# Kernel tuning notes

Hardware: AMD Instinct MI355X
Metric: run time of the kernel (lower is better)

Reference implementation:

```python
import jax, jax.numpy as jnp
import numpy as np

D_MODEL = 512
DQ = D_MODEL // 4  # 128
TIME_SHIFT_START = 256
VELOCITY_START = 768
NOTE_OFF_START = 128


def conv1d(x, w, b, stride, pad):
    # x: [B, Cin, L], w: [Cout, Cin, K]
    y = jax.lax.conv_general_dilated(x, w, (stride,), [(pad, pad)],
                                     dimension_numbers=('NCH', 'OIH', 'NCH'))
    return y + b[None, :, None]


def adaptive_avg_pool1d(x, out_size):
    # faithful to torch AdaptiveAvgPool1d bin boundaries
    L = x.shape[-1]
    starts = (np.arange(out_size) * L) // out_size
    ends = np.ceil((np.arange(out_size) + 1) * L / out_size).astype(np.int64)
    cs = jnp.concatenate([jnp.zeros(x.shape[:-1] + (1,), x.dtype),
                          jnp.cumsum(x, axis=-1)], axis=-1)
    return (cs[..., ends] - cs[..., starts]) / jnp.asarray(ends - starts, x.dtype)


def setup_inputs() -> dict:
    key = jax.random.key(0)
    ks = jax.random.split(key, 20)

    def w(k, shape):
        fan_in = int(np.prod(shape[1:]))
        return jax.random.normal(k, shape, jnp.float32) / np.sqrt(fan_in)

    def b(k, n):
        return jax.random.normal(k, (n,), jnp.float32) * 0.01

    return {
        'tokens': jax.random.randint(ks[0], (32, 4096), 0, 774),
        'r1_w': w(ks[1], (32, 1, 8)),    'r1_b': b(ks[2], 32),
        'r2_w': w(ks[3], (64, 32, 4)),   'r2_b': b(ks[4], 64),
        'h1_w': w(ks[5], (64, 128, 12)), 'h1_b': b(ks[6], 64),
        'h2_w': w(ks[7], (32, 64, 8)),   'h2_b': b(ks[8], 32),
        'm1_w': w(ks[9], (64, 128, 5)),  'm1_b': b(ks[10], 64),
        'm2_w': w(ks[11], (32, 64, 3)),  'm2_b': b(ks[12], 32),
        'd1_w': w(ks[13], (16, 6, 4)),   'd1_b': b(ks[14], 16),
        'd2_w': w(ks[15], (16, 16, 3)),  'd2_b': b(ks[16], 16),
        'fc_w': w(ks[17], (D_MODEL, D_MODEL)), 'fc_b': b(ks[18], D_MODEL),
    }


def reference(tokens, r1_w, r1_b, r2_w, r2_b, h1_w, h1_b, h2_w, h2_b,
              m1_w, m1_b, m2_w, m2_b, d1_w, d1_b, d2_w, d2_b, fc_w, fc_b):
    B, S = tokens.shape
    relu = jax.nn.relu

    # rhythm: binary time-shift indicator [B,1,S]
    ts = ((tokens >= TIME_SHIFT_START) & (tokens < VELOCITY_START)).astype(jnp.float32)[:, None, :]
    r = relu(conv1d(ts, r1_w, r1_b, 2, 3))
    r = relu(conv1d(r, r2_w, r2_b, 2, 1))
    r = adaptive_avg_pool1d(r, DQ).reshape(B, -1)  # [B, 64*DQ]

    # vectorized one-hot pitch scatter (replaces the python double loop): [B,128,S]
    nm = tokens < NOTE_OFF_START
    pitch = jnp.transpose(
        jax.nn.one_hot(jnp.where(nm, tokens, 0) % 128, 128, dtype=jnp.float32)
        * nm[..., None].astype(jnp.float32), (0, 2, 1))

    h = relu(conv1d(pitch, h1_w, h1_b, 1, 6))
    h = relu(conv1d(h, h2_w, h2_b, 2, 3))
    h = adaptive_avg_pool1d(h, DQ).reshape(B, -1)  # [B, 32*DQ]

    m = relu(conv1d(pitch, m1_w, m1_b, 1, 2))
    m = relu(conv1d(m, m2_w, m2_b, 1, 1))
    m = adaptive_avg_pool1d(m, DQ).reshape(B, -1)  # [B, 32*DQ]

    # velocity one-hot scatter: [B,6,S]
    vm = tokens >= VELOCITY_START
    vel = jnp.clip(jnp.where(vm, tokens - VELOCITY_START, 0), 0, 5)
    vpat = jnp.transpose(
        jax.nn.one_hot(vel, 6, dtype=jnp.float32) * vm[..., None].astype(jnp.float32),
        (0, 2, 1))
    d = relu(conv1d(vpat, d1_w, d1_b, 1, 2))
    d = relu(conv1d(d, d2_w, d2_b, 1, 1))
    d = adaptive_avg_pool1d(d, DQ).reshape(B, -1)  # [B, 16*DQ]

    # total flattened size is 36*d_model != d_model, so torch branch always pools
    r, h, m, d = [adaptive_avg_pool1d(f[:, None, :], DQ)[:, 0] for f in (r, h, m, d)]

    combined = jnp.concatenate([r, h, m, d], axis=1)       # [B, d_model]
    feats = combined @ fc_w.T + fc_b                        # Linear
    return jnp.broadcast_to(feats[:, None, :], (B, S, D_MODEL))
```

## Files before the change

### kernel.cpp

```cpp
#include <hip/hip_runtime.h>

typedef unsigned short u16;
typedef unsigned int u32;
typedef float vf4 __attribute__((ext_vector_type(4)));
typedef unsigned int vu4 __attribute__((ext_vector_type(4)));
typedef short sh8 __attribute__((ext_vector_type(8)));
typedef float f32x4 __attribute__((ext_vector_type(4)));

__device__ __forceinline__ float bf2f(u16 u) {
  return __uint_as_float(((u32)u) << 16);
}
__device__ __forceinline__ u16 f2bf(float f) {
  u32 x = __float_as_uint(f);
  return (u16)((x + 0x7fffu + ((x >> 16) & 1u)) >> 16);
}
__device__ __forceinline__ float ldin(const void* p, int idx, int isf) {
  return isf ? ((const float*)p)[idx] : bf2f(((const u16*)p)[idx]);
}

#define OFF_FLAG  ((size_t)0)
#define OFF_WB    ((size_t)16)
#define OFF_WTH1  ((size_t)1180432)
#define OFF_WTM1  ((size_t)1576720)
#define OFF_COMB  ((size_t)1741840)
#define OFF_FEATF ((size_t)1807376)
#define OFF_FEATB ((size_t)1872912)
#define OFF_DP    ((size_t)18686736)
#define OFF_WH2B  ((size_t)52536080)
#define OFF_WH2L  ((size_t)52568848)
#define OFF_WM2B  ((size_t)52601616)
#define OFF_WM2L  ((size_t)52613904)
#define WS_NEEDED ((size_t)52626192)

#define WB_R1W 0
#define WB_R1B 256
#define WB_R2W 288
#define WB_R2B 8480
#define WB_H1B 8544
#define WB_H2W 8608
#define WB_H2B 24992
#define WB_M1B 25024
#define WB_M2W 25088
#define WB_M2B 31232
#define WB_D1W 31264
#define WB_D1B 31648
#define WB_D2W 31664
#define WB_D2B 32432
#define WB_FCW 32448
#define WB_FCB 294592
#define WB_TOTAL 295104

#define CV_TH1_END 394176
#define CV_TM1_END 435456
#define CV_CMB_END 451840
#define CV_WH2_END 468224
#define CV_TOTAL   474368

__global__ __launch_bounds__(256) void k_convert(
    const void* r1_w, const void* r1_b, const void* r2_w, const void* r2_b,
    const void* h1_w, const void* h1_b, const void* h2_w, const void* h2_b,
    const void* m1_w, const void* m1_b, const void* m2_w, const void* m2_b,
    const void* d1_w, const void* d1_b, const void* d2_w, const void* d2_b,
    const void* fc_w, const void* fc_b,
    int* __restrict__ flagp, float* __restrict__ wb,
    float* __restrict__ wTh1, float* __restrict__ wTm1,
    float* __restrict__ combined,
    u16* __restrict__ wh2b, u16* __restrict__ wh2l,
    u16* __restrict__ wm2b, u16* __restrict__ wm2l) {
  __shared__ int cnt[4];
  int tid = threadIdx.x;
  {
    u16 v = ((const u16*)fc_w)[2 * tid];
    int e = (v >> 7) & 0xFF;
    int outside = (e < 100 || e > 140) ? 1 : 0;
    unsigned long long m = __ballot(outside);
    if ((tid & 63) == 0) cnt[tid >> 6] = __popcll(m);
  }
  __syncthreads();
  int isf = (cnt[0] + cnt[1] + cnt[2] + cnt[3] >= 64) ? 1 : 0;
  if (blockIdx.x == 0 && tid == 0) flagp[0] = isf;

  int j = blockIdx.x * 256 + tid;
  if (j >= CV_TOTAL) return;
  if (j < WB_TOTAL) {
    const void* src; int si;
    if      (j < WB_R1B) { src = r1_w; si = j; }
    else if (j < WB_R2W) { src = r1_b; si = j - WB_R1B; }
    else if (j < WB_R2B) { src = r2_w; si = j - WB_R2W; }
    else if (j < WB_H1B) { src = r2_b; si = j - WB_R2B; }
    else if (j < WB_H2W) { src = h1_b; si = j - WB_H1B; }
    else if (j < WB_H2B) { src = h2_w; si = j - WB_H2W; }
    else if (j < WB_M1B) { src = h2_b; si = j - WB_H2B; }
    else if (j < WB_M2W) { src = m1_b; si = j - WB_M1B; }
    else if (j < WB_M2B) { src = m2_w; si = j - WB_M2W; }
    else if (j < WB_D1W) { src = m2_b; si = j - WB_M2B; }
    else if (j < WB_D1B) { src = d1_w; si = j - WB_D1W; }
    else if (j < WB_D2W) { src = d1_b; si = j - WB_D1B; }
    else if (j < WB_D2B) { src = d2_w; si = j - WB_D2W; }
    else if (j < WB_FCW) { src = d2_b; si = j - WB_D2B; }
    else if (j < WB_FCB) { src = fc_w; si = j - WB_FCW; }
    else                 { src = fc_b; si = j - WB_FCB; }
    wb[j] = ldin(src, si, isf);
  } else if (j < CV_TH1_END) {
    int j2 = j - WB_TOTAL;
    int o = j2 & 63, r = j2 >> 6;
    wTh1[j2] = (r >= 1536) ? 0.f : ldin(h1_w, (o * 128 + r / 12) * 12 + (r % 12), isf);
  } else if (j < CV_TM1_END) {
    int j3 = j - CV_TH1_END;
    int o = j3 & 63, r = j3 >> 6;
    wTm1[j3] = (r >= 640) ? 0.f : ldin(m1_w, (o * 128 + r / 5) * 5 + (r % 5), isf);
  } else if (j < CV_CMB_END) {
    combined[j - CV_TM1_END] = 0.f;
  } else if (j < CV_WH2_END) {
    int jj = j - CV_CMB_END;
    int o = jj >> 9, rem = jj & 511, c = rem >> 3, kk = rem & 7;
    float w = ldin(h2_w, (o * 64 + c) * 8 + kk, isf);
    u16 hi = f2bf(w);
    wh2b[jj] = hi;
    wh2l[jj] = f2bf(w - bf2f(hi));
  } else {
    int jj = j - CV_WH2_END;
    int kk = jj >> 11, rem = jj & 2047, o = rem >> 6, c = rem & 63;
    float w = ldin(m2_w, (o * 64 + c) * 3 + kk, isf);
    u16 hi = f2bf(w);
    wm2b[jj] = hi;
    wm2l[jj] = f2bf(w - bf2f(hi));
  }
}


#define HT_STRIDE 142
#define MT2_STRIDE 72

__device__ __forceinline__ void dev_hf(float* smem, const int* tok,
                                       const float* wTh1, const float* h1bf,
                                       const u16* wh2b, const u16* wh2l,
                                       const float* h2bf,
                                       float* combined, int chunk, int q, int b) {
  u16* htile = (u16*)smem;
  int* tks = (int*)(smem + 4544);
  const int tid = threadIdx.x;
  const int tb = q * 512 + chunk * 64;
  const int sg0 = 2 * tb;
  const int* tokb = tok + b * 4096;
  if (tid < 146) {
    int x = sg0 - 9 + tid;
    int p = ((unsigned)x < 4096u) ? tokb[x] : 128;
    tks[tid] = (p < 128 ? p : 128) * 768;
  }
  __syncthreads();
  {
    const int og = tid & 15, slot = tid >> 4;
    const float4 bias = *(const float4*)(h1bf + og * 4);
    const float* wbase = wTh1 + og * 4;
    for (int pos = slot; pos < 134; pos += 16) {
      int t = sg0 - 3 + pos;
      u16 o0 = 0, o1 = 0, o2 = 0, o3 = 0;
      if ((unsigned)t <= 4096u) {
        float4 acc = bias;
#pragma unroll
        for (int k = 0; k < 12; ++k) {
          const float4 wv = *(const float4*)(wbase + tks[pos + k] + k * 64);
          acc.x += wv.x; acc.y += wv.y; acc.z += wv.z; acc.w += wv.w;
        }
        o0 = f2bf(fmaxf(acc.x, 0.f)); o1 = f2bf(fmaxf(acc.y, 0.f));
        o2 = f2bf(fmaxf(acc.z, 0.f)); o3 = f2bf(fmaxf(acc.w, 0.f));
      }
      int rb = og * 4 * HT_STRIDE + pos;
      htile[rb] = o0;
      htile[rb + HT_STRIDE] = o1;
      htile[rb + 2 * HT_STRIDE] = o2;
      htile[rb + 3 * HT_STRIDE] = o3;
    }
  }
  __syncthreads();
  const int w = tid >> 6, l = tid & 63;
  const int quad = l >> 4, n = l & 15;
  const int ot = w & 1, tp = w >> 1;
  f32x4 acc2[2];
  acc2[0] = (f32x4){0.f, 0.f, 0.f, 0.f};
  acc2[1] = (f32x4){0.f, 0.f, 0.f, 0.f};
  const u16* wph = wh2b + (size_t)(16 * ot + n) * 512 + quad * 8;
  const u16* wpl = wh2l + (size_t)(16 * ot + n) * 512 + quad * 8;
  const u32* hp = (const u32*)htile;
  for (int kc = 0; kc < 2; ++kc) {
    sh8 ah[8], al[8];
#pragma unroll
    for (int s = 0; s < 8; ++s) {
      ah[s] = *(const sh8*)(wph + kc * 256 + 32 * s);
      al[s] = *(const sh8*)(wpl + kc * 256 + 32 * s);
    }
#pragma unroll
    for (int it = 0; it < 2; ++it) {
      int fb = 16 * (2 * it + tp) + n;
#pragma unroll
      for (int s = 0; s < 8; ++s) {
        int c = kc * 32 + 4 * s + quad;
        const u32* p = hp + c * 71 + fb;
        u32 bw[4] = {p[0], p[1], p[2], p[3]};
        sh8 bb;
        __builtin_memcpy(&bb, bw, 16);
        acc2[it] = __builtin_amdgcn_mfma_f32_16x16x32_bf16(ah[s], bb, acc2[it], 0, 0, 0);
        acc2[it] = __builtin_amdgcn_mfma_f32_16x16x32_bf16(al[s], bb, acc2[it], 0, 0, 0);
      }
    }
  }
#pragma unroll
  for (int r = 0; r < 4; ++r) {
    float bsv = h2bf[16 * ot + quad * 4 + r];
    float s = fmaxf(acc2[0][r] + bsv, 0.f) + fmaxf(acc2[1][r] + bsv, 0.f);
    s += __shfl_xor(s, 1, 64);
    s += __shfl_xor(s, 2, 64);
    s += __shfl_xor(s, 4, 64);
    s += __shfl_xor(s, 8, 64);
    if (n == 0) {
      int o = 16 * ot + quad * 4 + r;
      atomicAdd(&combined[b * 512 + 128 + 4 * o + q], s * (1.f / 512.f));
    }
  }
}

__device__ __forceinline__ void dev_mf(float* smem, const int* tok,
                                       const float* wTm1, const float* m1bf,
                                       const u16* wm2b, const u16* wm2l,
                                       const float* m2bf,
                                       float* combined, int sub, int q, int b) {
  u16* mT = (u16*)smem;
  int* tks = (int*)(smem + 4716);
  const int tid = threadIdx.x;
  const int tb = q * 1024 + sub * 128;
  const int* tokb = tok + b * 4096;
  if (tid < 135) {
    int x = tb - 4 + tid;
    int p = ((unsigned)x < 4096u) ? tokb[x] : 128;
    tks[tid] = (p < 128 ? p : 128) * 320;
  }
  __syncthreads();
  {
    const int og = tid & 15, slot = tid >> 4;
    const float4 bias = *(const float4*)(m1bf + og * 4);
    const float* wbase = wTm1 + og * 4;
    for (int u = slot; u < 131; u += 16) {
      int t = tb - 2 + u;
      u16 o0 = 0, o1 = 0, o2 = 0, o3 = 0;
      if ((unsigned)t < 4096u) {
        float4 acc = bias;
#pragma unroll
        for (int k = 0; k < 5; ++k) {
          const float4 wv = *(const float4*)(wbase + tks[u + k] + k * 64);
          acc.x += wv.x; acc.y += wv.y; acc.z += wv.z; acc.w += wv.w;
        }
        o0 = f2bf(fmaxf(acc.x, 0.f)); o1 = f2bf(fmaxf(acc.y, 0.f));
        o2 = f2bf(fmaxf(acc.z, 0.f)); o3 = f2bf(fmaxf(acc.w, 0.f));
      }
      uint2 pack;
      pack.x = (u32)o0 | ((u32)o1 << 16);
      pack.y = (u32)o2 | ((u32)o3 << 16);
      *(uint2*)&mT[u * MT2_STRIDE + og * 4] = pack;
    }
  }
  __syncthreads();
  const int w = tid >> 6, l = tid & 63;
  const int quad = l >> 4, n = l & 15;
  const int ot = w & 1, tp = w >> 1;
  sh8 ah[3][2], al[3][2];
  {
    const u16* wph = wm2b + (size_t)(16 * ot + n) * 64 + quad * 8;
    const u16* wpl = wm2l + (size_t)(16 * ot + n) * 64 + quad * 8;
#pragma unroll
    for (int kk = 0; kk < 3; ++kk) {
#pragma unroll
      for (int kc = 0; kc < 2; ++kc) {
        ah[kk][kc] = *(const sh8*)(wph + kk * 2048 + kc * 32);
        al[kk][kc] = *(const sh8*)(wpl + kk * 2048 + kc * 32);
      }
    }
  }
  float bsv[4];
#pragma unroll
  for (int r = 0; r < 4; ++r) bsv[r] = m2bf[16 * ot + quad * 4 + r];
  float sm[4] = {0.f, 0.f, 0.f, 0.f};
  for (int it = 0; it < 4; ++it) {
    const int un = 16 * (2 * it + tp) + n + 1;
    f32x4 acc = {0.f, 0.f, 0.f, 0.f};
#pragma unroll
    for (int kk = 0; kk < 3; ++kk) {
      const u16* rowp = mT + (un + kk) * MT2_STRIDE + quad * 8;
#pragma unroll
      for (int kc = 0; kc < 2; ++kc) {
        sh8 bb = *(const sh8*)(rowp + kc * 32);
        acc = __builtin_amdgcn_mfma_f32_16x16x32_bf16(ah[kk][kc], bb, acc, 0, 0, 0);
        acc = __builtin_amdgcn_mfma_f32_16x16x32_bf16(al[kk][kc], bb, acc, 0, 0, 0);
      }
    }
#pragma unroll
    for (int r = 0; r < 4; ++r) sm[r] += fmaxf(acc[r] + bsv[r], 0.f);
  }
#pragma unroll
  for (int r = 0; r < 4; ++r) {
    float s = sm[r];
    s += __shfl_xor(s, 1, 64);
    s += __shfl_xor(s, 2, 64);
    s += __shfl_xor(s, 4, 64);
    s += __shfl_xor(s, 8, 64);
    if (n == 0) {
      int o = 16 * ot + quad * 4 + r;
      atomicAdd(&combined[b * 512 + 256 + 4 * o + q], s * (1.f / 1024.f));
    }
  }
}

__device__ __forceinline__ void dev_rf(float* smem, const int* tok,
                                       const float* r1wf, const float* r1bf,
                                       const float* r2wf, const float* r2bf,
                                       float* combined, int chunk, int b) {
  float* w1s = smem;
  float* b1s = smem + 256;
  float* Ibuf = smem + 288;
  float* r1t = smem + 560;
  float* wcr = smem + 4848;
  const int tid = threadIdx.x;
  const int tbase = chunk * 64;
  const int tk0 = 4 * tbase - 7;
  const int* tokb = tok + b * 4096;
  w1s[tid] = r1wf[tid];
  if (tid < 32) b1s[tid] = r1bf[tid];
  for (int i = tid; i < 270; i += 256) {
    int x = tk0 + i;
    float v = 0.f;
    if ((unsigned)x < 4096u) {
      int tk = tokb[x];
      v = (tk >= 256 && tk < 768) ? 1.f : 0.f;
    }
    Ibuf[i] = v;
  }
  __syncthreads();
  {
    const int tl1 = tid & 63, og1 = tid >> 6;
    for (int xi = tl1; xi < 134; xi += 64) {
      int x = 2 * tbase - 2 + xi;
      if ((unsigned)x < 2048u) {
        float iv[8];
#pragma unroll
        for (int k = 0; k < 8; ++k) iv[k] = Ibuf[2 * xi + k];
#pragma unroll
        for (int i = 0; i < 8; ++i) {
          int o = og1 * 8 + i;
          float a = b1s[o];
#pragma unroll
          for (int k = 0; k < 8; ++k) a = fmaf(w1s[o * 8 + k], iv[k], a);
          r1t[o * 134 + xi] = fmaxf(a, 0.f);
        }
      } else {
#pragma unroll
        for (int i = 0; i < 8; ++i) r1t[(og1 * 8 + i) * 134 + xi] = 0.f;
      }
    }
  }
  __syncthreads();
  const int half = chunk >> 3;
  const int og = tid >> 6, tl = tid & 63;
  float acc[16];
#pragma unroll
  for (int i = 0; i < 16; ++i) acc[i] = 0.f;
  for (int c0 = 0; c0 < 32; c0 += 8) {
    for (int f = tid; f < 2048; f += 256) {
      int o = f & 63, r = f >> 6, k = r & 3, cc = r >> 2;
      wcr[f] = r2wf[(o * 32 + c0 + cc) * 4 + k];
    }
    __syncthreads();
#pragma unroll
    for (int cc = 0; cc < 8; ++cc) {
      const float* rr = r1t + (c0 + cc) * 134 + 2 * tl;
      float ev[3], od[3];
#pragma unroll
      for (int f3 = 0; f3 < 3; ++f3) {
        ev[f3] = rr[2 * f3];
        od[f3] = rr[2 * f3 + 1];
      }
#pragma unroll
      for (int k = 0; k < 4; ++k) {
        const int p = (k + 1) & 1, fk = (k + 1) >> 1;
        const float* wv = &wcr[(cc * 4 + k) * 64 + og * 16];
        float4 wa = *(const float4*)wv;
        float4 wbv = *(const float4*)(wv + 4);
        float4 wcc = *(const float4*)(wv + 8);
        float4 wd4 = *(const float4*)(wv + 12);
        float wr[16] = {wa.x, wa.y, wa.z, wa.w, wbv.x, wbv.y, wbv.z, wbv.w,
                        wcc.x, wcc.y, wcc.z, wcc.w, wd4.x, wd4.y, wd4.z, wd4.w};
        float v0 = p ? od[fk] : ev[fk];
#pragma unroll
        for (int i = 0; i < 16; ++i) acc[i] = fmaf(v0, wr[i], acc[i]);
      }
    }
    __syncthreads();
  }
  const float inv = 1.f / 512.f;
#pragma unroll
  for (int i = 0; i < 16; ++i) {
    int o = og * 16 + i;
    float s = fmaxf(acc[i] + r2bf[o], 0.f);
#pragma unroll
    for (int d = 32; d > 0; d >>= 1) s += __shfl_down(s, d, 64);
    if (tl == 0) atomicAdd(&combined[b * 512 + 2 * o + half], s * inv);
  }
}

__device__ __forceinline__ void dev_df(float* smem, const int* tok,
                                       const float* d1wf, const float* d1bf,
                                       const float* d2wf, const float* d2bf,
                                       float* dpws, int chunk, int b) {
  float* wds7 = smem;
  float* wd = smem + 448;
  int* cls = (int*)(smem + 1216);
  float (*dt)[132] = reinterpret_cast<float(*)[132]>(smem + 1352);
  float* c2 = smem + 3464;
  const int tid = threadIdx.x;
  const int tbase = chunk * 128;
  const int* tokb = tok + b * 4096;
  for (int f = tid; f < 448; f += 256) {
    int k = f & 3, rest = f >> 2, v = rest % 7, c = rest / 7;
    wds7[f] = (v < 6) ? d1wf[(c * 6 + v) * 4 + k] : 0.f;
  }
  for (int f = tid; f < 768; f += 256) wd[f] = d2wf[f];
  if (tid < 136) {
    int x = tbase - 3 + tid;
    int v = 6;
    if ((unsigned)x < 4096u) {
      int tk = tokb[x];
      if (tk >= 768) { v = tk - 768; v = v > 5 ? 5 : v; } else v = 6;
    }
    cls[tid] = v;
  }
  __syncthreads();
  for (int f = tid; f < 16 * 131; f += 256) {
    int iu = f % 131, c = f / 131;
    int x = tbase - 1 + iu;
    float v = 0.f;
    if (x >= 0 && x <= 4096) {
      float a = d1bf[c];
#pragma unroll
      for (int k = 0; k < 4; ++k) {
        a += wds7[(c * 7 + cls[iu + k]) * 4 + k];
      }
      v = fmaxf(a, 0.f);
    }
    dt[c][iu] = v;
  }
  __syncthreads();
  for (int idx = tid; idx < 16 * 129; idx += 256) {
    int o = idx / 129, tl = idx % 129;
    float a = d2bf[o];
    const float* ww = &wd[o * 48];
#pragma unroll 4
    for (int c = 0; c < 16; ++c) {
      a = fmaf(dt[c][tl], ww[c * 3 + 0],
          fmaf(dt[c][tl + 1], ww[c * 3 + 1],
          fmaf(dt[c][tl + 2], ww[c * 3 + 2], a)));
    }
    c2[o * 133 + tl] = fmaxf(a, 0.f);
  }
  __syncthreads();
  if (tid < 64) {
    int o = tid >> 2, qq = tid & 3;
    const float* row = c2 + o * 133 + 32 * qq;
    float s = 0.f;
#pragma unroll
    for (int j = 0; j < 33; ++j) s += row[j];
    dpws[(size_t)(b * 16 + o) * 128 + 4 * chunk + qq] = s * (1.f / 33.f);
  }
}

__global__ __launch_bounds__(256, 4) void k_fused(const int* __restrict__ tok,
                                                  const float* __restrict__ wb,
                                                  const float* __restrict__ wTh1,
                                                  const float* __restrict__ wTm1,
                                                  const u16* __restrict__ wh2b,
                                                  const u16* __restrict__ wh2l,
                                                  const u16* __restrict__ wm2b,
                                                  const u16* __restrict__ wm2l,
                                                  float* __restrict__ combined,
                                                  float* __restrict__ dpws) {
  __shared__ __align__(16) float smem[6896];
  int bx = blockIdx.x;
  if (bx < 1024) {
    dev_hf(smem, tok, wTh1, wb + WB_H1B, wh2b, wh2l, wb + WB_H2B, combined,
           bx & 7, (bx >> 3) & 3, bx >> 5);
  } else if (bx < 2048) {
    int n = bx - 1024;
    dev_mf(smem, tok, wTm1, wb + WB_M1B, wm2b, wm2l, wb + WB_M2B, combined,
           n & 7, (n >> 3) & 3, n >> 5);
  } else if (bx < 2560) {
    int n = bx - 2048;
    dev_rf(smem, tok, wb + WB_R1W, wb + WB_R1B, wb + WB_R2W, wb + WB_R2B,
           combined, n & 15, n >> 4);
  } else {
    int n = bx - 2560;
    dev_df(smem, tok, wb + WB_D1W, wb + WB_D1B, wb + WB_D2W, wb + WB_D2B,
           dpws, n & 31, n >> 5);
  }
}

__global__ __launch_bounds__(256) void k_fc(const float* __restrict__ combined,
                                            const float* __restrict__ dpws,
                                            const float* __restrict__ fcwf,
                                            const float* __restrict__ fcbf,
                                            float* __restrict__ featf,
                                            u16* __restrict__ featb) {
  const int bx = blockIdx.x;
  const int b = bx >> 3, oct = bx & 7;
  const int tid = threadIdx.x;
  __shared__ float cb[512];
  cb[tid] = combined[b * 512 + tid];
  if (tid < 128) {
    cb[256 + tid] = combined[b * 512 + 256 + tid];
  } else {
    int j = tid - 128;
    int o = j >> 3, i0 = (j & 7) * 16;
    const float* row = dpws + (size_t)(b * 16 + o) * 128;
    float s = 0.f;
#pragma unroll
    for (int i = 0; i < 16; ++i) s += row[i0 + i];
    cb[384 + j] = s * (1.f / 16.f);
  }
  __syncthreads();
  const int oo = oct * 64 + (tid >> 2), part = tid & 3;
  float acc = 0.f;
  const float4* wr = (const float4*)(fcwf + (size_t)oo * 512 + part * 128);
#pragma unroll 8
  for (int j4 = 0; j4 < 32; ++j4) {
    float4 w = wr[j4];
    const float* c4 = &cb[part * 128 + j4 * 4];
    acc = fmaf(c4[0], w.x, acc);
    acc = fmaf(c4[1], w.y, acc);
    acc = fmaf(c4[2], w.z, acc);
    acc = fmaf(c4[3], w.w, acc);
  }
  acc += __shfl_xor(acc, 1, 64);
  acc += __shfl_xor(acc, 2, 64);
  if (part == 0) {
    float r = acc + fcbf[oo];
    featf[b * 512 + oo] = r;
    featb[b * 512 + oo] = f2bf(r);
  }
}

__global__ __launch_bounds__(256) void k_bcast(const int* __restrict__ flagp,
                                               const vf4* __restrict__ featf4,
                                               const vu4* __restrict__ featb4,
                                               vf4* __restrict__ outf,
                                               vu4* __restrict__ outb) {
  if (flagp[0]) {
    int base = blockIdx.x * 1024 + threadIdx.x;
#pragma unroll
    for (int s = 0; s < 4; ++s) {
      int g = base + s * 256;
      vf4 v = featf4[(g >> 19) * 128 + (g & 127)];
      __builtin_nontemporal_store(v, &outf[g]);
    }
  } else {
    int base = blockIdx.x * 512 + threadIdx.x;
#pragma unroll
    for (int s = 0; s < 2; ++s) {
      int g = base + s * 256;
      vu4 v = featb4[(g >> 18) * 64 + (g & 63)];
      __builtin_nontemporal_store(v, &outb[g]);
    }
  }
}

extern "C" void kernel_launch(void* const* d_in, const int* in_sizes, int n_in,
                              void* d_out, int out_size, void* d_ws, size_t ws_size,
                              hipStream_t stream) {
  if (ws_size < WS_NEEDED) return;

  const int* tokens = (const int*)d_in[0];
  const void* r1_w = d_in[1];  const void* r1_b = d_in[2];
  const void* r2_w = d_in[3];  const void* r2_b = d_in[4];
  const void* h1_w = d_in[5];  const void* h1_b = d_in[6];
  const void* h2_w = d_in[7];  const void* h2_b = d_in[8];
  const void* m1_w = d_in[9];  const void* m1_b = d_in[10];
  const void* m2_w = d_in[11]; const void* m2_b = d_in[12];
  const void* d1_w = d_in[13]; const void* d1_b = d_in[14];
  const void* d2_w = d_in[15]; const void* d2_b = d_in[16];
  const void* fc_w = d_in[17]; const void* fc_b = d_in[18];

  char* ws = (char*)d_ws;
  int*   flagp   = (int*)  (ws + OFF_FLAG);
  float* wb      = (float*)(ws + OFF_WB);
  float* wTh1    = (float*)(ws + OFF_WTH1);
  float* wTm1    = (float*)(ws + OFF_WTM1);
  float* combined= (float*)(ws + OFF_COMB);
  float* featf   = (float*)(ws + OFF_FEATF);
  u16*   featb   = (u16*)  (ws + OFF_FEATB);
  float* dpws    = (float*)(ws + OFF_DP);
  u16*   wh2b    = (u16*)  (ws + OFF_WH2B);
  u16*   wh2l    = (u16*)  (ws + OFF_WH2L);
  u16*   wm2b    = (u16*)  (ws + OFF_WM2B);
  u16*   wm2l    = (u16*)  (ws + OFF_WM2L);

  k_convert<<<1853, 256, 0, stream>>>(r1_w, r1_b, r2_w, r2_b, h1_w, h1_b, h2_w, h2_b,
                                      m1_w, m1_b, m2_w, m2_b, d1_w, d1_b, d2_w, d2_b,
                                      fc_w, fc_b, flagp, wb, wTh1, wTm1, combined,
                                      wh2b, wh2l, wm2b, wm2l);
  k_fused<<<3584, 256, 0, stream>>>(tokens, wb, wTh1, wTm1, wh2b, wh2l, wm2b, wm2l,
                                    combined, dpws);
  k_fc<<<256, 256, 0, stream>>>(combined, dpws, wb + WB_FCW, wb + WB_FCB, featf, featb);
  k_bcast<<<16384, 256, 0, stream>>>(flagp, (const vf4*)featf, (const vu4*)featb,
                                     (vf4*)d_out, (vu4*)d_out);
}
```

Baseline: 391.3 us.

## Fuse FC and output broadcast into a single kernel

Merges the linear layer and the broadcast write into one kernel. Each block computes the full 512-wide feature vector for its batch row in shared memory and then streams 512 sequence rows of output. This removes one kernel launch and the global feature round-trip, at the cost of recomputing the FC per block and launching far fewer blocks for the large output write.

```diff
diff --git a/kernel.cpp b/kernel.cpp
--- a/kernel.cpp
+++ b/kernel.cpp
@@ -23,8 +23,6 @@
 #define OFF_WTH1  ((size_t)1180432)
 #define OFF_WTM1  ((size_t)1576720)
 #define OFF_COMB  ((size_t)1741840)
-#define OFF_FEATF ((size_t)1807376)
-#define OFF_FEATB ((size_t)1872912)
 #define OFF_DP    ((size_t)18686736)
 #define OFF_WH2B  ((size_t)52536080)
 #define OFF_WH2L  ((size_t)52568848)
@@ -501,16 +499,19 @@
   }
 }
 
-__global__ __launch_bounds__(256) void k_fc(const float* __restrict__ combined,
-                                            const float* __restrict__ dpws,
-                                            const float* __restrict__ fcwf,
-                                            const float* __restrict__ fcbf,
-                                            float* __restrict__ featf,
-                                            u16* __restrict__ featb) {
+__global__ __launch_bounds__(256) void k_out(const int* __restrict__ flagp,
+                                             const float* __restrict__ combined,
+                                             const float* __restrict__ dpws,
+                                             const float* __restrict__ fcwf,
+                                             const float* __restrict__ fcbf,
+                                             float* __restrict__ outf,
+                                             u16* __restrict__ outb) {
   const int bx = blockIdx.x;
-  const int b = bx >> 3, oct = bx & 7;
+  const int b = bx >> 3, rc = bx & 7;
   const int tid = threadIdx.x;
   __shared__ float cb[512];
+  __shared__ __align__(16) float feat[512];
+  __shared__ __align__(16) u32 featu[256];
   cb[tid] = combined[b * 512 + tid];
   if (tid < 128) {
     cb[256 + tid] = combined[b * 512 + 256 + tid];
@@ -524,47 +525,41 @@
     cb[384 + j] = s * (1.f / 16.f);
   }
   __syncthreads();
-  const int oo = oct * 64 + (tid >> 2), part = tid & 3;
-  float acc = 0.f;
-  const float4* wr = (const float4*)(fcwf + (size_t)oo * 512 + part * 128);
+  for (int h = 0; h < 2; ++h) {
+    int oo = h * 256 + tid;
+    float acc = fcbf[oo];
+    const float4* wr = (const float4*)(fcwf + (size_t)oo * 512);
 #pragma unroll 8
-  for (int j4 = 0; j4 < 32; ++j4) {
-    float4 w = wr[j4];
-    const float* c4 = &cb[part * 128 + j4 * 4];
-    acc = fmaf(c4[0], w.x, acc);
-    acc = fmaf(c4[1], w.y, acc);
-    acc = fmaf(c4[2], w.z, acc);
-    acc = fmaf(c4[3], w.w, acc);
-  }
-  acc += __shfl_xor(acc, 1, 64);
-  acc += __shfl_xor(acc, 2, 64);
-  if (part == 0) {
-    float r = acc + fcbf[oo];
-    featf[b * 512 + oo] = r;
-    featb[b * 512 + oo] = f2bf(r);
-  }
-}
-
-__global__ __launch_bounds__(256) void k_bcast(const int* __restrict__ flagp,
-                                               const vf4* __restrict__ featf4,
-                                               const vu4* __restrict__ featb4,
-                                               vf4* __restrict__ outf,
-                                               vu4* __restrict__ outb) {
+    for (int j4 = 0; j4 < 128; ++j4) {
+      float4 w = wr[j4];
+      const float* c4 = &cb[j4 * 4];
+      acc = fmaf(c4[0], w.x, acc);
+      acc = fmaf(c4[1], w.y, acc);
+      acc = fmaf(c4[2], w.z, acc);
+      acc = fmaf(c4[3], w.w, acc);
+    }
+    feat[oo] = acc;
+  }
+  __syncthreads();
+  featu[tid] = (u32)f2bf(feat[2 * tid]) | ((u32)f2bf(feat[2 * tid + 1]) << 16);
+  __syncthreads();
+  const int lane = tid & 63, w = tid >> 6;
+  const size_t rowbase = (size_t)b * 4096 + (size_t)rc * 512;
   if (flagp[0]) {
-    int base = blockIdx.x * 1024 + threadIdx.x;
-#pragma unroll
-    for (int s = 0; s < 4; ++s) {
-      int g = base + s * 256;
-      vf4 v = featf4[(g >> 19) * 128 + (g & 127)];
-      __builtin_nontemporal_store(v, &outf[g]);
+    const vf4* f4 = (const vf4*)feat;
+    vf4 v0 = f4[lane];
+    vf4 v1 = f4[lane + 64];
+    for (int r = w; r < 512; r += 4) {
+      vf4* op = (vf4*)(outf + (rowbase + r) * 512);
+      __builtin_nontemporal_store(v0, op + lane);
+      __builtin_nontemporal_store(v1, op + lane + 64);
     }
   } else {
-    int base = blockIdx.x * 512 + threadIdx.x;
-#pragma unroll
-    for (int s = 0; s < 2; ++s) {
-      int g = base + s * 256;
-      vu4 v = featb4[(g >> 18) * 64 + (g & 63)];
-      __builtin_nontemporal_store(v, &outb[g]);
+    const vu4* f4 = (const vu4*)featu;
+    vu4 v0 = f4[lane];
+    for (int r = w; r < 512; r += 4) {
+      vu4* op = (vu4*)(outb + (rowbase + r) * 512);
+      __builtin_nontemporal_store(v0, op + lane);
     }
   }
 }
@@ -591,8 +586,6 @@
   float* wTh1    = (float*)(ws + OFF_WTH1);
   float* wTm1    = (float*)(ws + OFF_WTM1);
   float* combined= (float*)(ws + OFF_COMB);
-  float* featf   = (float*)(ws + OFF_FEATF);
-  u16*   featb   = (u16*)  (ws + OFF_FEATB);
   float* dpws    = (float*)(ws + OFF_DP);
   u16*   wh2b    = (u16*)  (ws + OFF_WH2B);
   u16*   wh2l    = (u16*)  (ws + OFF_WH2L);
@@ -605,7 +598,6 @@
                                       wh2b, wh2l, wm2b, wm2l);
   k_fused<<<3584, 256, 0, stream>>>(tokens, wb, wTh1, wTm1, wh2b, wh2l, wm2b, wm2l,
                                     combined, dpws);
-  k_fc<<<256, 256, 0, stream>>>(combined, dpws, wb + WB_FCW, wb + WB_FCB, featf, featb);
-  k_bcast<<<16384, 256, 0, stream>>>(flagp, (const vf4*)featf, (const vu4*)featb,
-                                     (vf4*)d_out, (vu4*)d_out);
-}
+  k_out<<<256, 256, 0, stream>>>(flagp, combined, dpws, wb + WB_FCW, wb + WB_FCB,
+                                 (float*)d_out, (u16*)d_out);
+}
```

After: 417.3 us. +6.6%, slower.
